# Kernel tuning notes

Hardware: AMD Instinct MI355X
Metric: run time of the kernel (lower is better)

Reference implementation:

```python
import jax, jax.numpy as jnp
import numpy as np

ITEM_NUM = 1_000_000
MAXLEN = 200
H = 128
NH = 2
NB = 2
B = 2048
FLOAT_MIN = -1000.0
EPS = 1e-8


def _ln(x, g, b):
    mu = jnp.mean(x, axis=-1, keepdims=True)
    var = jnp.mean((x - mu) ** 2, axis=-1, keepdims=True)
    return (x - mu) / jnp.sqrt(var + EPS) * g + b


def setup_inputs() -> dict:
    key = jax.random.key(0)
    ks = jax.random.split(key, 32)
    s = 1.0 / np.sqrt(H)
    d = {}
    d['user_ids'] = jax.random.randint(ks[0], (B,), 0, 100000)
    d['log_seqs'] = jax.random.randint(ks[1], (B, MAXLEN), 0, ITEM_NUM)
    d['pos_seqs'] = jax.random.randint(ks[2], (B, MAXLEN), 0, ITEM_NUM)
    d['neg_seqs'] = jax.random.randint(ks[3], (B, MAXLEN), 0, ITEM_NUM)
    item = jax.random.normal(ks[4], (ITEM_NUM + 1, H), jnp.float32) * 0.02
    d['item_table'] = item.at[0].set(0.0)  # padding_idx=0
    pos = jax.random.normal(ks[5], (MAXLEN + 1, H), jnp.float32) * 0.02
    d['pos_table'] = pos.at[0].set(0.0)
    # per-block stacked params, torch Linear layout [out,in]
    d['qw'] = jax.random.normal(ks[6], (NB, H, H), jnp.float32) * s
    d['kw'] = jax.random.normal(ks[7], (NB, H, H), jnp.float32) * s
    d['vw'] = jax.random.normal(ks[8], (NB, H, H), jnp.float32) * s
    d['ow'] = jax.random.normal(ks[9], (NB, H, H), jnp.float32) * s
    d['qb'] = jnp.zeros((NB, H), jnp.float32)
    d['kb'] = jnp.zeros((NB, H), jnp.float32)
    d['vb'] = jnp.zeros((NB, H), jnp.float32)
    d['ob'] = jnp.zeros((NB, H), jnp.float32)
    d['w1'] = jax.random.normal(ks[10], (NB, H, H), jnp.float32) * s  # conv1 k=1 == linear
    d['b1'] = jnp.zeros((NB, H), jnp.float32)
    d['w2'] = jax.random.normal(ks[11], (NB, H, H), jnp.float32) * s
    d['b2'] = jnp.zeros((NB, H), jnp.float32)
    d['ln1_g'] = jnp.ones((NB, H), jnp.float32)
    d['ln1_b'] = jnp.zeros((NB, H), jnp.float32)
    d['ln2_g'] = jnp.ones((NB, H), jnp.float32)
    d['ln2_b'] = jnp.zeros((NB, H), jnp.float32)
    d['lnf_g'] = jnp.ones((H,), jnp.float32)
    d['lnf_b'] = jnp.zeros((H,), jnp.float32)
    return d


def reference(item_table, pos_table, qw, qb, kw, kb, vw, vb, ow, ob,
              ln1_g, ln1_b, w1, b1, w2, b2, ln2_g, ln2_b, lnf_g, lnf_b,
              user_ids, log_seqs, pos_seqs, neg_seqs):
    Bb, L = log_seqs.shape
    hd = H // NH
    seqs = item_table[log_seqs] * jnp.asarray(np.sqrt(H), jnp.float32)  # [B,L,H]
    poss = jnp.arange(1, L + 1)[None, :] * (log_seqs != 0)
    seqs = seqs + pos_table[poss]
    causal = jnp.triu(jnp.ones((L, L), bool), k=1)  # True = masked (future)
    for i in range(NB):
        x = seqs
        Q = (x @ qw[i].T + qb[i]).reshape(Bb, L, NH, hd).transpose(0, 2, 1, 3)
        K = (x @ kw[i].T + kb[i]).reshape(Bb, L, NH, hd).transpose(0, 2, 1, 3)
        V = (x @ vw[i].T + vb[i]).reshape(Bb, L, NH, hd).transpose(0, 2, 1, 3)
        scores = jnp.einsum('bhqd,bhkd->bhqk', Q, K) / jnp.asarray(np.sqrt(hd), jnp.float32)
        scores = jnp.where(causal, FLOAT_MIN, scores)
        attn_w = jax.nn.softmax(scores, axis=-1)
        attn = jnp.einsum('bhqk,bhkd->bhqd', attn_w, V)
        attn = attn.transpose(0, 2, 1, 3).reshape(Bb, L, H)
        mha = attn @ ow[i].T + ob[i]
        seqs = _ln(x + mha, ln1_g[i], ln1_b[i])
        ff = jax.nn.relu(seqs @ w1[i].T + b1[i]) @ w2[i].T + b2[i]
        seqs = _ln(seqs + ff, ln2_g[i], ln2_b[i])
    log_feats = _ln(seqs, lnf_g, lnf_b)
    pos_logits = jnp.sum(log_feats * item_table[pos_seqs], axis=-1)
    neg_logits = jnp.sum(log_feats * item_table[neg_seqs], axis=-1)
    return (pos_logits, neg_logits)
```

## Files before the change

### kernel.cpp

```cpp
#include <hip/hip_runtime.h>
#include <math.h>

#define L 200
#define H 128
#define HD 64
#define NB 2
#define BTOT 2048
#define HH (H * H)
#define XSS 136

typedef short bf16x8 __attribute__((ext_vector_type(8)));
typedef float f32x4 __attribute__((ext_vector_type(4)));
typedef unsigned short u16;

#define MFMA16 __builtin_amdgcn_mfma_f32_16x16x32_bf16

__device__ __forceinline__ u16 f2bf(float f) {
    unsigned u = __builtin_bit_cast(unsigned, f);
    u = u + 0x7fffu + ((u >> 16) & 1u);
    return (u16)(u >> 16);
}
__device__ __forceinline__ float bf2f(u16 s) {
    return __builtin_bit_cast(float, ((unsigned)s) << 16);
}
__device__ __forceinline__ bf16x8 pack8(float4 a, float4 b, float sc) {
    bf16x8 r;
    r[0] = (short)f2bf(a.x * sc); r[1] = (short)f2bf(a.y * sc);
    r[2] = (short)f2bf(a.z * sc); r[3] = (short)f2bf(a.w * sc);
    r[4] = (short)f2bf(b.x * sc); r[5] = (short)f2bf(b.y * sc);
    r[6] = (short)f2bf(b.z * sc); r[7] = (short)f2bf(b.w * sc);
    return r;
}

__global__ __launch_bounds__(256) void cvt_kernel(const float* __restrict__ src,
                                                  u16* __restrict__ dst, int n8) {
    int i = blockIdx.x * 256 + threadIdx.x;
    if (i >= n8) return;
    float4 a0 = ((const float4*)src)[i * 2];
    float4 a1 = ((const float4*)src)[i * 2 + 1];
    ((bf16x8*)dst)[i] = pack8(a0, a1, 1.0f);
}

__global__ __launch_bounds__(256) void embed_kernel(const int* __restrict__ ids,
                                                    const float4* __restrict__ item,
                                                    const float4* __restrict__ post,
                                                    u16* __restrict__ X, int M) {
    int idx = blockIdx.x * 256 + threadIdx.x;
    if (idx >= M * 16) return;
    int r = idx >> 4, c8 = idx & 15;
    int id = ids[r];
    int l = r % L;
    int p = (id != 0) ? (l + 1) : 0;
    float4 a0 = item[(size_t)id * 32 + c8 * 2];
    float4 a1 = item[(size_t)id * 32 + c8 * 2 + 1];
    float4 p0 = post[(size_t)p * 32 + c8 * 2];
    float4 p1 = post[(size_t)p * 32 + c8 * 2 + 1];
    const float sc = 11.313708498984761f;
    float4 o0 = make_float4(a0.x * sc + p0.x, a0.y * sc + p0.y, a0.z * sc + p0.z, a0.w * sc + p0.w);
    float4 o1 = make_float4(a1.x * sc + p1.x, a1.y * sc + p1.y, a1.z * sc + p1.z, a1.w * sc + p1.w);
    *(bf16x8*)&X[(size_t)r * 128 + c8 * 8] = pack8(o0, o1, 1.0f);
}

__global__ __launch_bounds__(256) void qkv_kernel(const u16* __restrict__ X,
        const u16* __restrict__ wq, const u16* __restrict__ wk, const u16* __restrict__ wv,
        const float* __restrict__ qb, const float* __restrict__ kb, const float* __restrict__ vb,
        u16* __restrict__ Qo, u16* __restrict__ Ko, u16* __restrict__ Vo, int M) {
    __shared__ u16 Xs[128 * XSS];
    __shared__ u16 Ot[4][16 * XSS];
    int tid = threadIdx.x, w = tid >> 6, lane = tid & 63, g = lane >> 4, l15 = lane & 15;
    int row0 = blockIdx.x * 128;
#pragma unroll
    for (int it = 0; it < 8; ++it) {
        int idx = it * 256 + tid;
        int r = idx >> 4, c8 = idx & 15;
        size_t gr = (size_t)min(row0 + r, M - 1);
        *(bf16x8*)&Xs[r * XSS + c8 * 8] = *(const bf16x8*)(X + gr * 128 + c8 * 8);
    }
    __syncthreads();

    int arow = w * 32 + l15;
    int ko = g * 8;

#pragma unroll
    for (int p = 0; p < 3; ++p) {
        const u16* Wp = p == 0 ? wq : (p == 1 ? wk : wv);
        const float* bp = p == 0 ? qb : (p == 1 ? kb : vb);
        u16* Op = p == 0 ? Qo : (p == 1 ? Ko : Vo);
        const float scale = p == 0 ? 0.125f : 1.0f;

        f32x4 acc[2][8];
#pragma unroll
        for (int nt = 0; nt < 8; ++nt) {
            float bv = bp[nt * 16 + l15];
            acc[0][nt] = (f32x4){bv, bv, bv, bv};
            acc[1][nt] = (f32x4){bv, bv, bv, bv};
        }
#pragma unroll
        for (int kc = 0; kc < 4; ++kc) {
            bf16x8 a0 = *(const bf16x8*)&Xs[arow * XSS + kc * 32 + ko];
            bf16x8 a1 = *(const bf16x8*)&Xs[(arow + 16) * XSS + kc * 32 + ko];
#pragma unroll
            for (int nt = 0; nt < 8; ++nt) {
                bf16x8 b = *(const bf16x8*)(Wp + ((size_t)(nt * 16 + l15) << 7) + kc * 32 + ko);
                acc[0][nt] = MFMA16(a0, b, acc[0][nt], 0, 0, 0);
                acc[1][nt] = MFMA16(a1, b, acc[1][nt], 0, 0, 0);
            }
        }
#pragma unroll
        for (int mt = 0; mt < 2; ++mt) {
#pragma unroll
            for (int r = 0; r < 4; ++r) {
                int ml = g * 4 + r;
#pragma unroll
                for (int nt = 0; nt < 8; ++nt)
                    Ot[w][ml * XSS + nt * 16 + l15] = f2bf(acc[mt][nt][r] * scale);
            }
            asm volatile("s_waitcnt lgkmcnt(0)" ::: "memory");
#pragma unroll
            for (int j = 0; j < 4; ++j) {
                int chunk = j * 64 + lane;
                int rr = chunk >> 4, c16 = chunk & 15;
                bf16x8 v = *(const bf16x8*)&Ot[w][rr * XSS + c16 * 8];
                int grow = row0 + w * 32 + mt * 16 + rr;
                if (grow < M) *(bf16x8*)(Op + (size_t)grow * 128 + c16 * 8) = v;
            }
            asm volatile("s_waitcnt lgkmcnt(0)" ::: "memory");
        }
    }
}

__global__ __launch_bounds__(256) void oproj_ffn1_kernel(const u16* __restrict__ A,
        const u16* __restrict__ Wo, const float* __restrict__ ob,
        const u16* __restrict__ Xres, const float* __restrict__ gma, const float* __restrict__ bta,
        const u16* __restrict__ W1, const float* __restrict__ b1f,
        u16* __restrict__ Xout, u16* __restrict__ F1, int M) {
    __shared__ u16 Xs[128 * XSS];
    __shared__ u16 Ot[4][16 * XSS];
    int tid = threadIdx.x, w = tid >> 6, lane = tid & 63, g = lane >> 4, l15 = lane & 15;
    int row0 = blockIdx.x * 128;
    int rw = row0 + w * 32;
    size_t ar0 = (size_t)min(rw + l15, M - 1) * 128;
    size_t ar1 = (size_t)min(rw + 16 + l15, M - 1) * 128;
    int ko = g * 8;

    f32x4 acc[2][8];
#pragma unroll
    for (int nt = 0; nt < 8; ++nt) {
        float bv = ob[nt * 16 + l15];
        acc[0][nt] = (f32x4){bv, bv, bv, bv};
        acc[1][nt] = (f32x4){bv, bv, bv, bv};
    }
#pragma unroll
    for (int kc = 0; kc < 4; ++kc) {
        bf16x8 a0 = *(const bf16x8*)(A + ar0 + kc * 32 + ko);
        bf16x8 a1 = *(const bf16x8*)(A + ar1 + kc * 32 + ko);
#pragma unroll
        for (int nt = 0; nt < 8; ++nt) {
            bf16x8 b = *(const bf16x8*)(Wo + ((size_t)(nt * 16 + l15) << 7) + kc * 32 + ko);
            acc[0][nt] = MFMA16(a0, b, acc[0][nt], 0, 0, 0);
            acc[1][nt] = MFMA16(a1, b, acc[1][nt], 0, 0, 0);
        }
    }
    float gg[8], bb[8];
#pragma unroll
    for (int nt = 0; nt < 8; ++nt) { gg[nt] = gma[nt * 16 + l15]; bb[nt] = bta[nt * 16 + l15]; }
#pragma unroll
    for (int mt = 0; mt < 2; ++mt) {
#pragma unroll
        for (int r = 0; r < 4; ++r) {
            int rowl = w * 32 + mt * 16 + g * 4 + r;
            size_t rb = (size_t)min(row0 + rowl, M - 1) * 128;
            float v[8];
            float s = 0.f;
#pragma unroll
            for (int nt = 0; nt < 8; ++nt) { v[nt] = acc[mt][nt][r] + bf2f(Xres[rb + nt * 16 + l15]); s += v[nt]; }
            s += __shfl_xor(s, 1); s += __shfl_xor(s, 2); s += __shfl_xor(s, 4); s += __shfl_xor(s, 8);
            float mean = s * 0.0078125f;
            float s2 = 0.f;
#pragma unroll
            for (int nt = 0; nt < 8; ++nt) { float d = v[nt] - mean; s2 += d * d; }
            s2 += __shfl_xor(s2, 1); s2 += __shfl_xor(s2, 2); s2 += __shfl_xor(s2, 4); s2 += __shfl_xor(s2, 8);
            float inv = rsqrtf(s2 * 0.0078125f + 1e-8f);
#pragma unroll
            for (int nt = 0; nt < 8; ++nt)
                Xs[rowl * XSS + nt * 16 + l15] = f2bf((v[nt] - mean) * inv * gg[nt] + bb[nt]);
        }
    }
    __syncthreads();

#pragma unroll
    for (int it = 0; it < 8; ++it) {
        int idx = it * 256 + tid;
        int r = idx >> 4, c8 = idx & 15;
        int grow = row0 + r;
        if (grow < M)
            *(bf16x8*)(Xout + (size_t)grow * 128 + c8 * 8) = *(const bf16x8*)&Xs[r * XSS + c8 * 8];
    }

    int arow = w * 32 + l15;
    f32x4 acc2[2][8];
#pragma unroll
    for (int nt = 0; nt < 8; ++nt) {
        float bv = b1f[nt * 16 + l15];
        acc2[0][nt] = (f32x4){bv, bv, bv, bv};
        acc2[1][nt] = (f32x4){bv, bv, bv, bv};
    }
#pragma unroll
    for (int kc = 0; kc < 4; ++kc) {
        bf16x8 a0 = *(const bf16x8*)&Xs[arow * XSS + kc * 32 + ko];
        bf16x8 a1 = *(const bf16x8*)&Xs[(arow + 16) * XSS + kc * 32 + ko];
#pragma unroll
        for (int nt = 0; nt < 8; ++nt) {
            bf16x8 b = *(const bf16x8*)(W1 + ((size_t)(nt * 16 + l15) << 7) + kc * 32 + ko);
            acc2[0][nt] = MFMA16(a0, b, acc2[0][nt], 0, 0, 0);
            acc2[1][nt] = MFMA16(a1, b, acc2[1][nt], 0, 0, 0);
        }
    }
#pragma unroll
    for (int mt = 0; mt < 2; ++mt) {
#pragma unroll
        for (int r = 0; r < 4; ++r) {
            int ml = g * 4 + r;
#pragma unroll
            for (int nt = 0; nt < 8; ++nt)
                Ot[w][ml * XSS + nt * 16 + l15] = f2bf(fmaxf(acc2[mt][nt][r], 0.f));
        }
        asm volatile("s_waitcnt lgkmcnt(0)" ::: "memory");
#pragma unroll
        for (int j = 0; j < 4; ++j) {
            int chunk = j * 64 + lane;
            int rr = chunk >> 4, c16 = chunk & 15;
            bf16x8 v = *(const bf16x8*)&Ot[w][rr * XSS + c16 * 8];
            int grow = row0 + w * 32 + mt * 16 + rr;
            if (grow < M) *(bf16x8*)(F1 + (size_t)grow * 128 + c16 * 8) = v;
        }
        asm volatile("s_waitcnt lgkmcnt(0)" ::: "memory");
    }
}

__global__ __launch_bounds__(256) void ffn2_ln_kernel(const u16* __restrict__ A,
        const u16* __restrict__ W2, const float* __restrict__ bias,
        const u16* __restrict__ Xres, const float* __restrict__ gma, const float* __restrict__ bta,
        const float* __restrict__ gf, const float* __restrict__ bff, int fin,
        u16* __restrict__ Xout, const float* __restrict__ item,
        const int* __restrict__ pid, const int* __restrict__ nid,
        float* __restrict__ out, int gofs, int M) {
    __shared__ u16 Ot[4][16 * XSS];
    int tid = threadIdx.x, w = tid >> 6, lane = tid & 63, g = lane >> 4, l15 = lane & 15;
    int row0 = blockIdx.x * 128;
    int rw = row0 + w * 32;
    size_t ar0 = (size_t)min(rw + l15, M - 1) * 128;
    size_t ar1 = (size_t)min(rw + 16 + l15, M - 1) * 128;
    int ko = g * 8;

    f32x4 acc[2][8];
#pragma unroll
    for (int nt = 0; nt < 8; ++nt) {
        float bv = bias[nt * 16 + l15];
        acc[0][nt] = (f32x4){bv, bv, bv, bv};
        acc[1][nt] = (f32x4){bv, bv, bv, bv};
    }
#pragma unroll
    for (int kc = 0; kc < 4; ++kc) {
        bf16x8 a0 = *(const bf16x8*)(A + ar0 + kc * 32 + ko);
        bf16x8 a1 = *(const bf16x8*)(A + ar1 + kc * 32 + ko);
#pragma unroll
        for (int nt = 0; nt < 8; ++nt) {
            bf16x8 b = *(const bf16x8*)(W2 + ((size_t)(nt * 16 + l15) << 7) + kc * 32 + ko);
            acc[0][nt] = MFMA16(a0, b, acc[0][nt], 0, 0, 0);
            acc[1][nt] = MFMA16(a1, b, acc[1][nt], 0, 0, 0);
        }
    }
    float gg[8], bb[8], gg2[8], bb2[8];
#pragma unroll
    for (int nt = 0; nt < 8; ++nt) {
        gg[nt] = gma[nt * 16 + l15]; bb[nt] = bta[nt * 16 + l15];
        gg2[nt] = gf[nt * 16 + l15]; bb2[nt] = bff[nt * 16 + l15];
    }
#pragma unroll
    for (int mt = 0; mt < 2; ++mt) {
#pragma unroll
        for (int r = 0; r < 4; ++r) {
            int row = row0 + w * 32 + mt * 16 + g * 4 + r;
            size_t rb = (size_t)min(row, M - 1) * 128;
            float v[8];
            float s = 0.f;
#pragma unroll
            for (int nt = 0; nt < 8; ++nt) { v[nt] = acc[mt][nt][r] + bf2f(Xres[rb + nt * 16 + l15]); s += v[nt]; }
            s += __shfl_xor(s, 1); s += __shfl_xor(s, 2); s += __shfl_xor(s, 4); s += __shfl_xor(s, 8);
            float mean = s * 0.0078125f;
            float s2 = 0.f;
#pragma unroll
            for (int nt = 0; nt < 8; ++nt) { float d = v[nt] - mean; s2 += d * d; }
            s2 += __shfl_xor(s2, 1); s2 += __shfl_xor(s2, 2); s2 += __shfl_xor(s2, 4); s2 += __shfl_xor(s2, 8);
            float inv = rsqrtf(s2 * 0.0078125f + 1e-8f);
#pragma unroll
            for (int nt = 0; nt < 8; ++nt) v[nt] = (v[nt] - mean) * inv * gg[nt] + bb[nt];
            if (fin) {
                float t = 0.f;
#pragma unroll
                for (int nt = 0; nt < 8; ++nt) t += v[nt];
                t += __shfl_xor(t, 1); t += __shfl_xor(t, 2); t += __shfl_xor(t, 4); t += __shfl_xor(t, 8);
                float mean2 = t * 0.0078125f;
                float t2 = 0.f;
#pragma unroll
                for (int nt = 0; nt < 8; ++nt) { float d = v[nt] - mean2; t2 += d * d; }
                t2 += __shfl_xor(t2, 1); t2 += __shfl_xor(t2, 2); t2 += __shfl_xor(t2, 4); t2 += __shfl_xor(t2, 8);
                float inv2 = rsqrtf(t2 * 0.0078125f + 1e-8f);
#pragma unroll
                for (int nt = 0; nt < 8; ++nt) v[nt] = (v[nt] - mean2) * inv2 * gg2[nt] + bb2[nt];
                int gr = gofs + row;
                const float* prow = item + (size_t)pid[gr] * 128;
                const float* nrow = item + (size_t)nid[gr] * 128;
                float sp = 0.f, sn = 0.f;
#pragma unroll
                for (int nt = 0; nt < 8; ++nt) {
                    sp += v[nt] * prow[nt * 16 + l15];
                    sn += v[nt] * nrow[nt * 16 + l15];
                }
                sp += __shfl_xor(sp, 1); sp += __shfl_xor(sp, 2); sp += __shfl_xor(sp, 4); sp += __shfl_xor(sp, 8);
                sn += __shfl_xor(sn, 1); sn += __shfl_xor(sn, 2); sn += __shfl_xor(sn, 4); sn += __shfl_xor(sn, 8);
                if (l15 == 0 && row < M) {
                    out[gr] = sp;
                    out[(size_t)BTOT * L + gr] = sn;
                }
            } else {
                int ml = g * 4 + r;
#pragma unroll
                for (int nt = 0; nt < 8; ++nt)
                    Ot[w][ml * XSS + nt * 16 + l15] = f2bf(v[nt]);
            }
        }
        if (!fin) {
            asm volatile("s_waitcnt lgkmcnt(0)" ::: "memory");
#pragma unroll
            for (int j = 0; j < 4; ++j) {
                int chunk = j * 64 + lane;
                int rr = chunk >> 4, c16 = chunk & 15;
                bf16x8 v = *(const bf16x8*)&Ot[w][rr * XSS + c16 * 8];
                int grow = row0 + w * 32 + mt * 16 + rr;
                if (grow < M) *(bf16x8*)(Xout + (size_t)grow * 128 + c16 * 8) = v;
            }
            asm volatile("s_waitcnt lgkmcnt(0)" ::: "memory");
        }
    }
}

__global__ __launch_bounds__(256, 2) void attn_mfma_kernel(u16* __restrict__ Q,
                                                           const u16* __restrict__ K,
                                                           const u16* __restrict__ V) {
    __shared__ u16 lds_s[64 * 264];
    int b = blockIdx.x >> 1;
    int h = blockIdx.x & 1;
    int tid = threadIdx.x;
    int w = tid >> 6;
    int lane = tid & 63;
    int g = lane >> 4;
    int l15 = lane & 15;

    const u16* Kb = K + ((size_t)b * L) * H + h * HD;
    const u16* Vb = V + ((size_t)b * L) * H + h * HD;
    u16* Qb = Q + ((size_t)b * L) * H + h * HD;

    {
        int d = tid & 63;
        int kq = tid >> 6;
#pragma unroll 8
        for (int it = 0; it < 64; ++it) {
            int k = it * 4 + kq;
            lds_s[d * 264 + k] = Vb[(size_t)min(k, L - 1) * H + d];
        }
    }

    bf16x8 qf[4][2];
    int qrow[4];
#pragma unroll
    for (int nt = 0; nt < 4; ++nt) {
        int q = nt * 64 + w * 16 + l15;
        qrow[nt] = q;
        const u16* src = Qb + (size_t)min(q, L - 1) * H;
        qf[nt][0] = *(const bf16x8*)(src + g * 8);
        qf[nt][1] = *(const bf16x8*)(src + 32 + g * 8);
    }
    __syncthreads();

    f32x4 o[4][4];
    float mrun[4], lrun[4];
#pragma unroll
    for (int i = 0; i < 4; ++i) {
        mrun[i] = -1e30f; lrun[i] = 0.f;
#pragma unroll
        for (int j = 0; j < 4; ++j) o[i][j] = (f32x4){0.f, 0.f, 0.f, 0.f};
    }

    int rp = 8 * (l15 >> 2) + (l15 & 3);
    const f32x4 czero = {0.f, 0.f, 0.f, 0.f};

#pragma unroll
    for (int kc = 0; kc < 4; ++kc) {
        int kbase = kc * 64;
        bf16x8 ka[4][2];
#pragma unroll
        for (int mt = 0; mt < 4; ++mt) {
            int krow = kbase + (mt >> 1) * 32 + (mt & 1) * 4 + rp;
            const u16* src = Kb + (size_t)min(krow, L - 1) * H;
            ka[mt][0] = *(const bf16x8*)(src + g * 8);
            ka[mt][1] = *(const bf16x8*)(src + 32 + g * 8);
        }
#pragma unroll
        for (int nt = 0; nt < 4; ++nt) {
            if (nt < kc) continue;
            int q = qrow[nt];
            f32x4 c[4];
#pragma unroll
            for (int mt = 0; mt < 4; ++mt) {
                c[mt] = MFMA16(ka[mt][0], qf[nt][0], czero, 0, 0, 0);
                c[mt] = MFMA16(ka[mt][1], qf[nt][1], c[mt], 0, 0, 0);
            }
            float pm = -1e30f;
#pragma unroll
            for (int mt = 0; mt < 4; ++mt) {
#pragma unroll
                for (int r = 0; r < 4; ++r) {
                    int kact = kbase + 32 * (mt >> 1) + 4 * (mt & 1) + 8 * g + r;
                    float s = (kact <= q) ? c[mt][r] : -1e30f;
                    c[mt][r] = s;
                    pm = fmaxf(pm, s);
                }
            }
            pm = fmaxf(pm, __shfl_xor(pm, 16));
            pm = fmaxf(pm, __shfl_xor(pm, 32));
            float mnew = fmaxf(mrun[nt], pm);
            float sf = __expf(mrun[nt] - mnew);
            mrun[nt] = mnew;
            float ps = 0.f;
#pragma unroll
            for (int mt = 0; mt < 4; ++mt) {
#pragma unroll
                for (int r = 0; r < 4; ++r) {
                    float p = __expf(c[mt][r] - mnew);
                    c[mt][r] = p;
                    ps += p;
                }
            }
            ps += __shfl_xor(ps, 16);
            ps += __shfl_xor(ps, 32);
            lrun[nt] = lrun[nt] * sf + ps;
#pragma unroll
            for (int md = 0; md < 4; ++md) {
#pragma unroll
                for (int r = 0; r < 4; ++r) o[md][nt][r] *= sf;
            }
#pragma unroll
            for (int ks = 0; ks < 2; ++ks) {
                bf16x8 pb;
#pragma unroll
                for (int j = 0; j < 8; ++j)
                    pb[j] = (short)f2bf(c[2 * ks + (j >> 2)][j & 3]);
#pragma unroll
                for (int md = 0; md < 4; ++md) {
                    const u16* vp = &lds_s[(md * 16 + l15) * 264 + kbase + ks * 32 + g * 8];
                    bf16x8 va = *(const bf16x8*)vp;
                    o[md][nt] = MFMA16(va, pb, o[md][nt], 0, 0, 0);
                }
            }
        }
    }

    __syncthreads();
    u16* Ot = lds_s;
#pragma unroll
    for (int nt = 0; nt < 4; ++nt) {
        float inv = 1.0f / lrun[nt];
        int q = qrow[nt];
        int sw = (q & 7) << 3;
#pragma unroll
        for (int md = 0; md < 4; ++md) {
            int d0 = md * 16 + g * 4;
            unsigned p0 = (unsigned)f2bf(o[md][nt][0] * inv) | ((unsigned)f2bf(o[md][nt][1] * inv) << 16);
            unsigned p1 = (unsigned)f2bf(o[md][nt][2] * inv) | ((unsigned)f2bf(o[md][nt][3] * inv) << 16);
            uint2 u; u.x = p0; u.y = p1;
            *(uint2*)&Ot[q * 64 + (d0 ^ sw)] = u;
        }
    }
    __syncthreads();
    {
        int d = tid & 63;
        for (int q = tid >> 6; q < L; q += 4)
            Qb[(size_t)q * H + d] = Ot[q * 64 + (d ^ ((q & 7) << 3))];
    }
}

extern "C" void kernel_launch(void* const* d_in, const int* in_sizes, int n_in,
                              void* d_out, int out_size, void* d_ws, size_t ws_size,
                              hipStream_t stream) {
    const int* log_seqs = (const int*)d_in[1];
    const int* pos_seqs = (const int*)d_in[2];
    const int* neg_seqs = (const int*)d_in[3];
    const float* item = (const float*)d_in[4];
    const float* post = (const float*)d_in[5];
    const float* qw = (const float*)d_in[6];
    const float* kw = (const float*)d_in[7];
    const float* vw = (const float*)d_in[8];
    const float* ow = (const float*)d_in[9];
    const float* qb = (const float*)d_in[10];
    const float* kb = (const float*)d_in[11];
    const float* vb = (const float*)d_in[12];
    const float* ob = (const float*)d_in[13];
    const float* w1 = (const float*)d_in[14];
    const float* b1 = (const float*)d_in[15];
    const float* w2 = (const float*)d_in[16];
    const float* b2 = (const float*)d_in[17];
    const float* ln1g = (const float*)d_in[18];
    const float* ln1b = (const float*)d_in[19];
    const float* ln2g = (const float*)d_in[20];
    const float* ln2b = (const float*)d_in[21];
    const float* lnfg = (const float*)d_in[22];
    const float* lnfb = (const float*)d_in[23];
    float* out = (float*)d_out;

    int cb = 512;
    while (cb > 8 && (size_t)cb * L * H * 8 + 12 * HH * 2 > ws_size) cb >>= 1;
    size_t nbe = (size_t)cb * L * H;
    u16* X16 = (u16*)d_ws;
    u16* Q16 = X16 + nbe;
    u16* K16 = Q16 + nbe;
    u16* V16 = K16 + nbe;
    u16* w16 = V16 + nbe;

    const float* wsrc[6] = {qw, kw, vw, ow, w1, w2};
    int n8 = NB * HH / 8;
    for (int t = 0; t < 6; ++t)
        cvt_kernel<<<(n8 + 255) / 256, 256, 0, stream>>>(wsrc[t], w16 + (size_t)t * NB * HH, n8);

    for (int b0 = 0; b0 < BTOT; b0 += cb) {
        int M = cb * L;
        int gblk = (M + 127) / 128;
        embed_kernel<<<(M * 16 + 255) / 256, 256, 0, stream>>>(log_seqs + (size_t)b0 * L,
                                                               (const float4*)item, (const float4*)post,
                                                               X16, M);
        for (int i = 0; i < NB; ++i) {
            size_t wo = (size_t)i * HH;
            int bofs = i * H;
            qkv_kernel<<<gblk, 256, 0, stream>>>(X16,
                    w16 + 0 * NB * HH + wo, w16 + 1 * NB * HH + wo, w16 + 2 * NB * HH + wo,
                    qb + bofs, kb + bofs, vb + bofs, Q16, K16, V16, M);
            attn_mfma_kernel<<<cb * 2, 256, 0, stream>>>(Q16, K16, V16);
            oproj_ffn1_kernel<<<gblk, 256, 0, stream>>>(Q16, w16 + 3 * NB * HH + wo, ob + bofs,
                    X16, ln1g + bofs, ln1b + bofs,
                    w16 + 4 * NB * HH + wo, b1 + bofs, X16, K16, M);
            ffn2_ln_kernel<<<gblk, 256, 0, stream>>>(K16, w16 + 5 * NB * HH + wo, b2 + bofs,
                    X16, ln2g + bofs, ln2b + bofs, lnfg, lnfb, (i == NB - 1) ? 1 : 0,
                    X16, item, pos_seqs, neg_seqs, out, b0 * L, M);
        }
    }
}
```

Baseline: 1.605 ms.

## Fuse QKV projection into causal attention kernel per batch element

```diff
diff --git a/kernel.cpp b/kernel.cpp
--- a/kernel.cpp
+++ b/kernel.cpp
@@ -10,6 +10,7 @@
 #define XSS 136
 
 typedef short bf16x8 __attribute__((ext_vector_type(8)));
+typedef short bf16x4 __attribute__((ext_vector_type(4)));
 typedef float f32x4 __attribute__((ext_vector_type(4)));
 typedef unsigned short u16;
 
@@ -30,6 +31,19 @@
     r[4] = (short)f2bf(b.x * sc); r[5] = (short)f2bf(b.y * sc);
     r[6] = (short)f2bf(b.z * sc); r[7] = (short)f2bf(b.w * sc);
     return r;
+}
+__device__ __forceinline__ bf16x8 ld_q8(const u16* p) {
+    bf16x4 lo = *(const bf16x4*)p;
+    bf16x4 hi = *(const bf16x4*)(p + 4);
+    bf16x8 r;
+    r[0] = lo[0]; r[1] = lo[1]; r[2] = lo[2]; r[3] = lo[3];
+    r[4] = hi[0]; r[5] = hi[1]; r[6] = hi[2]; r[7] = hi[3];
+    return r;
+}
+__device__ __forceinline__ float rsum16(float v) {
+    v += __shfl_xor(v, 1); v += __shfl_xor(v, 2);
+    v += __shfl_xor(v, 4); v += __shfl_xor(v, 8);
+    return v;
 }
 
 __global__ __launch_bounds__(256) void cvt_kernel(const float* __restrict__ src,
@@ -61,71 +75,190 @@
     *(bf16x8*)&X[(size_t)r * 128 + c8 * 8] = pack8(o0, o1, 1.0f);
 }
 
-__global__ __launch_bounds__(256) void qkv_kernel(const u16* __restrict__ X,
-        const u16* __restrict__ wq, const u16* __restrict__ wk, const u16* __restrict__ wv,
-        const float* __restrict__ qb, const float* __restrict__ kb, const float* __restrict__ vb,
-        u16* __restrict__ Qo, u16* __restrict__ Ko, u16* __restrict__ Vo, int M) {
-    __shared__ u16 Xs[128 * XSS];
-    __shared__ u16 Ot[4][16 * XSS];
-    int tid = threadIdx.x, w = tid >> 6, lane = tid & 63, g = lane >> 4, l15 = lane & 15;
-    int row0 = blockIdx.x * 128;
-#pragma unroll
-    for (int it = 0; it < 8; ++it) {
-        int idx = it * 256 + tid;
-        int r = idx >> 4, c8 = idx & 15;
-        size_t gr = (size_t)min(row0 + r, M - 1);
-        *(bf16x8*)&Xs[r * XSS + c8 * 8] = *(const bf16x8*)(X + gr * 128 + c8 * 8);
-    }
-    __syncthreads();
-
-    int arow = w * 32 + l15;
-    int ko = g * 8;
-
-#pragma unroll
-    for (int p = 0; p < 3; ++p) {
-        const u16* Wp = p == 0 ? wq : (p == 1 ? wk : wv);
-        const float* bp = p == 0 ? qb : (p == 1 ? kb : vb);
-        u16* Op = p == 0 ? Qo : (p == 1 ? Ko : Vo);
-        const float scale = p == 0 ? 0.125f : 1.0f;
-
-        f32x4 acc[2][8];
-#pragma unroll
-        for (int nt = 0; nt < 8; ++nt) {
-            float bv = bp[nt * 16 + l15];
-            acc[0][nt] = (f32x4){bv, bv, bv, bv};
-            acc[1][nt] = (f32x4){bv, bv, bv, bv};
-        }
-#pragma unroll
-        for (int kc = 0; kc < 4; ++kc) {
-            bf16x8 a0 = *(const bf16x8*)&Xs[arow * XSS + kc * 32 + ko];
-            bf16x8 a1 = *(const bf16x8*)&Xs[(arow + 16) * XSS + kc * 32 + ko];
-#pragma unroll
-            for (int nt = 0; nt < 8; ++nt) {
-                bf16x8 b = *(const bf16x8*)(Wp + ((size_t)(nt * 16 + l15) << 7) + kc * 32 + ko);
-                acc[0][nt] = MFMA16(a0, b, acc[0][nt], 0, 0, 0);
-                acc[1][nt] = MFMA16(a1, b, acc[1][nt], 0, 0, 0);
+__global__ __launch_bounds__(512) void attnA_kernel(
+        const u16* __restrict__ X16,
+        const u16* __restrict__ Wq, const u16* __restrict__ Wk, const u16* __restrict__ Wv,
+        const float* __restrict__ qbp, const float* __restrict__ kbp, const float* __restrict__ vbp,
+        u16* __restrict__ O16) {
+    __shared__ u16 lds[39744];
+    u16* Ks = lds;
+    u16* Vt = lds + 14144;
+    u16* Qw = lds + 31040;
+    const int b = blockIdx.x;
+    const int tid = threadIdx.x;
+    const int w = tid >> 6, lane = tid & 63, g = lane >> 4, l15 = lane & 15;
+    const int rp = 8 * (l15 >> 2) + (l15 & 3);
+    const f32x4 czero = {0.f, 0.f, 0.f, 0.f};
+    const u16* Xb = X16 + (size_t)b * L * H;
+    u16* Ob = O16 + (size_t)b * L * H;
+    u16* qwp = Qw + w * 1088;
+
+    for (int idx = tid; idx < 64 * 56; idx += 512)
+        Vt[(idx / 56) * 264 + 208 + (idx % 56)] = 0;
+
+    const int ta = (w < 7) ? (12 - w) : -1;
+    const int tb = (w >= 1 && w < 7) ? (w - 1) : -1;
+
+    for (int h = 0; h < 2; ++h) {
+        for (int u = w; u < 26; u += 8) {
+            int rt = u >> 1;
+            int xr = min(rt * 16 + l15, L - 1);
+            bf16x8 xa[4];
+#pragma unroll
+            for (int kc = 0; kc < 4; ++kc)
+                xa[kc] = *(const bf16x8*)(Xb + (size_t)xr * H + kc * 32 + g * 8);
+            if (u & 1) {
+                f32x4 av[4];
+#pragma unroll
+                for (int dt = 0; dt < 4; ++dt) {
+                    float4 bv4 = *(const float4*)&vbp[h * 64 + dt * 16 + g * 4];
+                    av[dt] = (f32x4){bv4.x, bv4.y, bv4.z, bv4.w};
+                }
+#pragma unroll
+                for (int kc = 0; kc < 4; ++kc)
+#pragma unroll
+                    for (int dt = 0; dt < 4; ++dt) {
+                        bf16x8 wa = *(const bf16x8*)(Wv + (size_t)(h * 64 + dt * 16 + l15) * H + kc * 32 + g * 8);
+                        av[dt] = MFMA16(wa, xa[kc], av[dt], 0, 0, 0);
+                    }
+#pragma unroll
+                for (int dt = 0; dt < 4; ++dt)
+#pragma unroll
+                    for (int r = 0; r < 4; ++r)
+                        Vt[(dt * 16 + g * 4 + r) * 264 + rt * 16 + l15] = f2bf(av[dt][r]);
+            } else {
+                f32x4 ak[4];
+#pragma unroll
+                for (int ct = 0; ct < 4; ++ct) {
+                    float bv = kbp[h * 64 + ct * 16 + l15];
+                    ak[ct] = (f32x4){bv, bv, bv, bv};
+                }
+#pragma unroll
+                for (int kc = 0; kc < 4; ++kc)
+#pragma unroll
+                    for (int ct = 0; ct < 4; ++ct) {
+                        bf16x8 wb = *(const bf16x8*)(Wk + (size_t)(h * 64 + ct * 16 + l15) * H + kc * 32 + g * 8);
+                        ak[ct] = MFMA16(xa[kc], wb, ak[ct], 0, 0, 0);
+                    }
+#pragma unroll
+                for (int ct = 0; ct < 4; ++ct)
+#pragma unroll
+                    for (int r = 0; r < 4; ++r)
+                        Ks[(rt * 16 + g * 4 + r) * 68 + ct * 16 + l15] = f2bf(ak[ct][r]);
             }
         }
-#pragma unroll
-        for (int mt = 0; mt < 2; ++mt) {
-#pragma unroll
-            for (int r = 0; r < 4; ++r) {
-                int ml = g * 4 + r;
-#pragma unroll
-                for (int nt = 0; nt < 8; ++nt)
-                    Ot[w][ml * XSS + nt * 16 + l15] = f2bf(acc[mt][nt][r] * scale);
+        __syncthreads();
+
+#pragma unroll
+        for (int ti = 0; ti < 2; ++ti) {
+            int qt = ti ? tb : ta;
+            if (qt < 0) continue;
+            int qrow = qt * 16 + l15;
+            {
+                int xr = min(qrow, L - 1);
+                bf16x8 xa[4];
+#pragma unroll
+                for (int kc = 0; kc < 4; ++kc)
+                    xa[kc] = *(const bf16x8*)(Xb + (size_t)xr * H + kc * 32 + g * 8);
+                f32x4 aq[4];
+#pragma unroll
+                for (int dt = 0; dt < 4; ++dt) {
+                    float4 bv4 = *(const float4*)&qbp[h * 64 + dt * 16 + g * 4];
+                    aq[dt] = (f32x4){bv4.x, bv4.y, bv4.z, bv4.w};
+                }
+#pragma unroll
+                for (int kc = 0; kc < 4; ++kc)
+#pragma unroll
+                    for (int dt = 0; dt < 4; ++dt) {
+                        bf16x8 wa = *(const bf16x8*)(Wq + (size_t)(h * 64 + dt * 16 + l15) * H + kc * 32 + g * 8);
+                        aq[dt] = MFMA16(wa, xa[kc], aq[dt], 0, 0, 0);
+                    }
+#pragma unroll
+                for (int dt = 0; dt < 4; ++dt)
+#pragma unroll
+                    for (int i2 = 0; i2 < 2; ++i2) {
+                        unsigned pk = (unsigned)f2bf(aq[dt][2 * i2] * 0.125f) |
+                                      ((unsigned)f2bf(aq[dt][2 * i2 + 1] * 0.125f) << 16);
+                        *(unsigned*)&qwp[l15 * 68 + dt * 16 + g * 4 + 2 * i2] = pk;
+                    }
+                asm volatile("s_waitcnt lgkmcnt(0)" ::: "memory");
+                __builtin_amdgcn_sched_barrier(0);
             }
-            asm volatile("s_waitcnt lgkmcnt(0)" ::: "memory");
-#pragma unroll
-            for (int j = 0; j < 4; ++j) {
-                int chunk = j * 64 + lane;
-                int rr = chunk >> 4, c16 = chunk & 15;
-                bf16x8 v = *(const bf16x8*)&Ot[w][rr * XSS + c16 * 8];
-                int grow = row0 + w * 32 + mt * 16 + rr;
-                if (grow < M) *(bf16x8*)(Op + (size_t)grow * 128 + c16 * 8) = v;
+            bf16x8 qf0 = ld_q8(&qwp[l15 * 68 + g * 8]);
+            bf16x8 qf1 = ld_q8(&qwp[l15 * 68 + 32 + g * 8]);
+
+            f32x4 o2[4];
+#pragma unroll
+            for (int md = 0; md < 4; ++md) o2[md] = czero;
+            float mr = -1e30f, lr = 0.f;
+            int kcmax = qt >> 2;
+            for (int kc = 0; kc <= kcmax; ++kc) {
+                int kbase = kc * 64;
+                f32x4 c[4];
+#pragma unroll
+                for (int mt = 0; mt < 4; ++mt) {
+                    int krow = min(kbase + (mt >> 1) * 32 + (mt & 1) * 4 + rp, 207);
+                    bf16x8 ka0 = ld_q8(&Ks[krow * 68 + g * 8]);
+                    bf16x8 ka1 = ld_q8(&Ks[krow * 68 + 32 + g * 8]);
+                    c[mt] = MFMA16(ka0, qf0, czero, 0, 0, 0);
+                    c[mt] = MFMA16(ka1, qf1, c[mt], 0, 0, 0);
+                }
+                float pm = -1e30f;
+#pragma unroll
+                for (int mt = 0; mt < 4; ++mt)
+#pragma unroll
+                    for (int r = 0; r < 4; ++r) {
+                        int kact = kbase + 32 * (mt >> 1) + 4 * (mt & 1) + 8 * g + r;
+                        float s = (kact <= qrow) ? c[mt][r] : -1e30f;
+                        c[mt][r] = s;
+                        pm = fmaxf(pm, s);
+                    }
+                pm = fmaxf(pm, __shfl_xor(pm, 16));
+                pm = fmaxf(pm, __shfl_xor(pm, 32));
+                float mnew = fmaxf(mr, pm);
+                float sf = __expf(mr - mnew);
+                mr = mnew;
+                float ps = 0.f;
+#pragma unroll
+                for (int mt = 0; mt < 4; ++mt)
+#pragma unroll
+                    for (int r = 0; r < 4; ++r) {
+                        float p = __expf(c[mt][r] - mnew);
+                        c[mt][r] = p;
+                        ps += p;
+                    }
+                ps += __shfl_xor(ps, 16);
+                ps += __shfl_xor(ps, 32);
+                lr = lr * sf + ps;
+#pragma unroll
+                for (int md = 0; md < 4; ++md)
+#pragma unroll
+                    for (int r = 0; r < 4; ++r) o2[md][r] *= sf;
+#pragma unroll
+                for (int ks = 0; ks < 2; ++ks) {
+                    bf16x8 pb;
+#pragma unroll
+                    for (int j = 0; j < 8; ++j)
+                        pb[j] = (short)f2bf(c[2 * ks + (j >> 2)][j & 3]);
+#pragma unroll
+                    for (int md = 0; md < 4; ++md) {
+                        bf16x8 va = *(const bf16x8*)&Vt[(md * 16 + l15) * 264 + kbase + ks * 32 + g * 8];
+                        o2[md] = MFMA16(va, pb, o2[md], 0, 0, 0);
+                    }
+                }
             }
-            asm volatile("s_waitcnt lgkmcnt(0)" ::: "memory");
-        }
+            if (qrow < L) {
+                float inv = 1.0f / lr;
+#pragma unroll
+                for (int md = 0; md < 4; ++md) {
+                    unsigned p0 = (unsigned)f2bf(o2[md][0] * inv) | ((unsigned)f2bf(o2[md][1] * inv) << 16);
+                    unsigned p1 = (unsigned)f2bf(o2[md][2] * inv) | ((unsigned)f2bf(o2[md][3] * inv) << 16);
+                    uint2 uu; uu.x = p0; uu.y = p1;
+                    *(uint2*)(Ob + (size_t)qrow * H + h * 64 + md * 16 + g * 4) = uu;
+                }
+            }
+        }
+        __syncthreads();
     }
 }
 
@@ -343,151 +476,6 @@
             }
             asm volatile("s_waitcnt lgkmcnt(0)" ::: "memory");
         }
-    }
-}
-
-__global__ __launch_bounds__(256, 2) void attn_mfma_kernel(u16* __restrict__ Q,
-                                                           const u16* __restrict__ K,
-                                                           const u16* __restrict__ V) {
-    __shared__ u16 lds_s[64 * 264];
-    int b = blockIdx.x >> 1;
-    int h = blockIdx.x & 1;
-    int tid = threadIdx.x;
-    int w = tid >> 6;
-    int lane = tid & 63;
-    int g = lane >> 4;
-    int l15 = lane & 15;
-
-    const u16* Kb = K + ((size_t)b * L) * H + h * HD;
-    const u16* Vb = V + ((size_t)b * L) * H + h * HD;
-    u16* Qb = Q + ((size_t)b * L) * H + h * HD;
-
-    {
-        int d = tid & 63;
-        int kq = tid >> 6;
-#pragma unroll 8
-        for (int it = 0; it < 64; ++it) {
-            int k = it * 4 + kq;
-            lds_s[d * 264 + k] = Vb[(size_t)min(k, L - 1) * H + d];
-        }
-    }
-
-    bf16x8 qf[4][2];
-    int qrow[4];
-#pragma unroll
-    for (int nt = 0; nt < 4; ++nt) {
-        int q = nt * 64 + w * 16 + l15;
-        qrow[nt] = q;
-        const u16* src = Qb + (size_t)min(q, L - 1) * H;
-        qf[nt][0] = *(const bf16x8*)(src + g * 8);
-        qf[nt][1] = *(const bf16x8*)(src + 32 + g * 8);
-    }
-    __syncthreads();
-
-    f32x4 o[4][4];
-    float mrun[4], lrun[4];
-#pragma unroll
-    for (int i = 0; i < 4; ++i) {
-        mrun[i] = -1e30f; lrun[i] = 0.f;
-#pragma unroll
-        for (int j = 0; j < 4; ++j) o[i][j] = (f32x4){0.f, 0.f, 0.f, 0.f};
-    }
-
-    int rp = 8 * (l15 >> 2) + (l15 & 3);
-    const f32x4 czero = {0.f, 0.f, 0.f, 0.f};
-
-#pragma unroll
-    for (int kc = 0; kc < 4; ++kc) {
-        int kbase = kc * 64;
-        bf16x8 ka[4][2];
-#pragma unroll
-        for (int mt = 0; mt < 4; ++mt) {
-            int krow = kbase + (mt >> 1) * 32 + (mt & 1) * 4 + rp;
-            const u16* src = Kb + (size_t)min(krow, L - 1) * H;
-            ka[mt][0] = *(const bf16x8*)(src + g * 8);
-            ka[mt][1] = *(const bf16x8*)(src + 32 + g * 8);
-        }
-#pragma unroll
-        for (int nt = 0; nt < 4; ++nt) {
-            if (nt < kc) continue;
-            int q = qrow[nt];
-            f32x4 c[4];
-#pragma unroll
-            for (int mt = 0; mt < 4; ++mt) {
-                c[mt] = MFMA16(ka[mt][0], qf[nt][0], czero, 0, 0, 0);
-                c[mt] = MFMA16(ka[mt][1], qf[nt][1], c[mt], 0, 0, 0);
-            }
-            float pm = -1e30f;
-#pragma unroll
-            for (int mt = 0; mt < 4; ++mt) {
-#pragma unroll
-                for (int r = 0; r < 4; ++r) {
-                    int kact = kbase + 32 * (mt >> 1) + 4 * (mt & 1) + 8 * g + r;
-                    float s = (kact <= q) ? c[mt][r] : -1e30f;
-                    c[mt][r] = s;
-                    pm = fmaxf(pm, s);
-                }
-            }
-            pm = fmaxf(pm, __shfl_xor(pm, 16));
-            pm = fmaxf(pm, __shfl_xor(pm, 32));
-            float mnew = fmaxf(mrun[nt], pm);
-            float sf = __expf(mrun[nt] - mnew);
-            mrun[nt] = mnew;
-            float ps = 0.f;
-#pragma unroll
-            for (int mt = 0; mt < 4; ++mt) {
-#pragma unroll
-                for (int r = 0; r < 4; ++r) {
-                    float p = __expf(c[mt][r] - mnew);
-                    c[mt][r] = p;
-                    ps += p;
-                }
-            }
-            ps += __shfl_xor(ps, 16);
-            ps += __shfl_xor(ps, 32);
-            lrun[nt] = lrun[nt] * sf + ps;
-#pragma unroll
-            for (int md = 0; md < 4; ++md) {
-#pragma unroll
-                for (int r = 0; r < 4; ++r) o[md][nt][r] *= sf;
-            }
-#pragma unroll
-            for (int ks = 0; ks < 2; ++ks) {
-                bf16x8 pb;
-#pragma unroll
-                for (int j = 0; j < 8; ++j)
-                    pb[j] = (short)f2bf(c[2 * ks + (j >> 2)][j & 3]);
-#pragma unroll
-                for (int md = 0; md < 4; ++md) {
-                    const u16* vp = &lds_s[(md * 16 + l15) * 264 + kbase + ks * 32 + g * 8];
-                    bf16x8 va = *(const bf16x8*)vp;
-                    o[md][nt] = MFMA16(va, pb, o[md][nt], 0, 0, 0);
-                }
-            }
-        }
-    }
-
-    __syncthreads();
-    u16* Ot = lds_s;
-#pragma unroll
-    for (int nt = 0; nt < 4; ++nt) {
-        float inv = 1.0f / lrun[nt];
-        int q = qrow[nt];
-        int sw = (q & 7) << 3;
-#pragma unroll
-        for (int md = 0; md < 4; ++md) {
-            int d0 = md * 16 + g * 4;
-            unsigned p0 = (unsigned)f2bf(o[md][nt][0] * inv) | ((unsigned)f2bf(o[md][nt][1] * inv) << 16);
-            unsigned p1 = (unsigned)f2bf(o[md][nt][2] * inv) | ((unsigned)f2bf(o[md][nt][3] * inv) << 16);
-            uint2 u; u.x = p0; u.y = p1;
-            *(uint2*)&Ot[q * 64 + (d0 ^ sw)] = u;
-        }
-    }
-    __syncthreads();
-    {
-        int d = tid & 63;
-        for (int q = tid >> 6; q < L; q += 4)
-            Qb[(size_t)q * H + d] = Ot[q * 64 + (d ^ ((q & 7) << 3))];
     }
 }
 
@@ -527,6 +515,7 @@
     u16* K16 = Q16 + nbe;
     u16* V16 = K16 + nbe;
     u16* w16 = V16 + nbe;
+    (void)V16;
 
     const float* wsrc[6] = {qw, kw, vw, ow, w1, w2};
     int n8 = NB * HH / 8;
@@ -542,10 +531,9 @@
         for (int i = 0; i < NB; ++i) {
             size_t wo = (size_t)i * HH;
             int bofs = i * H;
-            qkv_kernel<<<gblk, 256, 0, stream>>>(X16,
+            attnA_kernel<<<cb, 512, 0, stream>>>(X16,
                     w16 + 0 * NB * HH + wo, w16 + 1 * NB * HH + wo, w16 + 2 * NB * HH + wo,
-                    qb + bofs, kb + bofs, vb + bofs, Q16, K16, V16, M);
-            attn_mfma_kernel<<<cb * 2, 256, 0, stream>>>(Q16, K16, V16);
+                    qb + bofs, kb + bofs, vb + bofs, Q16);
             oproj_ffn1_kernel<<<gblk, 256, 0, stream>>>(Q16, w16 + 3 * NB * HH + wo, ob + bofs,
                     X16, ln1g + bofs, ln1b + bofs,
                     w16 + 4 * NB * HH + wo, b1 + bofs, X16, K16, M);
```

New measurement: 1.761 ms. 1.1x slower.
